# Optimization experiments

Hardware: AMD Instinct MI355X
Metric: run time of the kernel (lower is better)

The kernel has to match this reference:

```python
import jax, jax.numpy as jnp
import numpy as np

B, S, H = 2, 2048, 2048
NH, NKV, HD = 16, 8, 128        # head_dim = H // NH
WINDOW = 1024                    # sliding window size
THETA = 100000.0                 # rope_theta (RotaryEmbedding base)


def setup_inputs() -> dict:
    key = jax.random.key(0)
    ks = jax.random.split(key, 5)
    hidden = jax.random.normal(ks[0], (B, S, H), jnp.float32)
    # fused QKV projection: [H, NH*HD + 2*NKV*HD]
    W_pack = jax.random.normal(ks[1], (H, NH * HD + 2 * NKV * HD), jnp.float32) * (H ** -0.5)
    W_o = jax.random.normal(ks[2], (NH * HD, H), jnp.float32) * ((NH * HD) ** -0.5)
    # per-KV-head 2-tap causal conv weights, softmax-normalized (as in nn.Parameter init)
    conv_k = jax.nn.softmax(jax.random.normal(ks[3], (NKV, 2), jnp.float32), axis=-1)
    conv_v = jax.nn.softmax(jax.random.normal(ks[4], (NKV, 2), jnp.float32), axis=-1)
    return {"hidden": hidden, "W_pack": W_pack, "W_o": W_o, "conv_k": conv_k, "conv_v": conv_v}


def _rope(x, cos, sin):
    # x: (b, s, h, d); cos/sin: (s, d//2); non-interleaved (rotate-half) form
    d2 = x.shape[-1] // 2
    x1, x2 = x[..., :d2], x[..., d2:]
    c = cos[None, :, None, :]
    s = sin[None, :, None, :]
    return jnp.concatenate([x1 * c - x2 * s, x2 * c + x1 * s], axis=-1)


def _causal_conv2(x, w):
    # x: (b, s, kv, d); w: (kv, 2). out[t] = w0*x[t-1] + w1*x[t], zero-padded at t=0
    x_prev = jnp.pad(x, ((0, 0), (1, 0), (0, 0), (0, 0)))[:, :-1]
    return w[None, None, :, 0:1] * x_prev + w[None, None, :, 1:2] * x


def reference(hidden, W_pack, W_o, conv_k, conv_v):
    b, s, _ = hidden.shape
    qkv = hidden @ W_pack                                  # (b, s, NH*HD + 2*NKV*HD)
    q = qkv[..., : NH * HD].reshape(b, s, NH, HD)
    k = qkv[..., NH * HD : NH * HD + NKV * HD].reshape(b, s, NKV, HD)
    v = qkv[..., NH * HD + NKV * HD :].reshape(b, s, NKV, HD)

    inv_freq = 1.0 / (THETA ** (jnp.arange(0, HD, 2, dtype=jnp.float32) / HD))
    freqs = jnp.outer(jnp.arange(s, dtype=jnp.float32), inv_freq)  # (s, HD/2)
    cos, sin = jnp.cos(freqs), jnp.sin(freqs)
    q = _rope(q, cos, sin)
    k = _rope(k, cos, sin)

    # learned 2-tap causal conv mixing adjacent K/V states, per KV head
    k = _causal_conv2(k, conv_k)
    v = _causal_conv2(v, conv_v)

    # GQA: repeat kv heads to match query heads
    group = NH // NKV
    k = jnp.repeat(k, group, axis=2)  # (b, s, NH, HD)
    v = jnp.repeat(v, group, axis=2)

    scores = jnp.einsum('bqhd,bkhd->bhqk', q, k) / jnp.sqrt(jnp.float32(HD))
    i = jnp.arange(s)[:, None]
    j = jnp.arange(s)[None, :]
    mask = (j <= i) & (i - j < WINDOW)  # causal sliding-window mask
    scores = jnp.where(mask[None, None], scores, jnp.finfo(scores.dtype).min)
    probs = jax.nn.softmax(scores, axis=-1)
    out = jnp.einsum('bhqk,bkhd->bqhd', probs, v).reshape(b, s, NH * HD)
    return out @ W_o
```

## Files before the change

kernel.cpp:

```cpp
#include <hip/hip_runtime.h>

#define DI __device__ __forceinline__

typedef unsigned short u16;
typedef __attribute__((ext_vector_type(8))) short s16x8;
typedef __attribute__((ext_vector_type(8))) unsigned short u16x8;
typedef __attribute__((ext_vector_type(4))) float f32x4;
typedef __attribute__((ext_vector_type(16))) float f32x16;

DI u16 f2bf(float x) {
  union { float f; unsigned u; } a; a.f = x;
  unsigned r = a.u + 0x7FFFu + ((a.u >> 16) & 1u);
  return (u16)(r >> 16);
}
DI float bf2f(u16 u) {
  union { unsigned u; float f; } a; a.u = ((unsigned)u) << 16;
  return a.f;
}
DI void gload16(const void* g, void* l) {
  __builtin_amdgcn_global_load_lds(
      (const __attribute__((address_space(1))) unsigned int*)g,
      (__attribute__((address_space(3))) unsigned int*)l, 16, 0, 0);
}
DI f32x4 mfma16(s16x8 a, s16x8 b, f32x4 c) {
  return __builtin_amdgcn_mfma_f32_16x16x32_bf16(a, b, c, 0, 0, 0);
}
DI f32x16 mfma32(s16x8 a, s16x8 b, f32x16 c) {
  return __builtin_amdgcn_mfma_f32_32x32x16_bf16(a, b, c, 0, 0, 0);
}

DI void store4(u16* p, f32x4 v) {
  union { u16 u[4]; unsigned long long ll; } o;
  o.u[0] = f2bf(v[0]); o.u[1] = f2bf(v[1]); o.u[2] = f2bf(v[2]); o.u[3] = f2bf(v[3]);
  *(unsigned long long*)p = o.ll;
}
DI void store4(float* p, f32x4 v) { *(f32x4*)p = v; }

#define SBAR() asm volatile("s_barrier" ::: "memory")

__global__ __launch_bounds__(256) void prep_kernel(
    const float* __restrict__ hidden, const float* __restrict__ W_pack,
    const float* __restrict__ W_o, u16* __restrict__ hA, u16* __restrict__ wpT,
    u16* __restrict__ woT, float* __restrict__ cosT, float* __restrict__ sinT) {
  int bi = blockIdx.x;
  int t = threadIdx.x;
  if (bi < 4096) {
    int i = bi * 256 + t;
    const float4* p = (const float4*)hidden + (size_t)i * 2;
    float4 a = p[0], b = p[1];
    u16x8 o;
    o[0] = f2bf(a.x); o[1] = f2bf(a.y); o[2] = f2bf(a.z); o[3] = f2bf(a.w);
    o[4] = f2bf(b.x); o[5] = f2bf(b.y); o[6] = f2bf(b.z); o[7] = f2bf(b.w);
    *((u16x8*)hA + i) = o;
  } else if (bi < 7168) {
    const float* W; u16* Wt; int R, C, c0, r0;
    if (bi < 6144) {
      int idx = bi - 4096;
      W = W_pack; Wt = wpT; R = 2048; C = 4096;
      c0 = (idx & 63) * 64; r0 = (idx >> 6) * 64;
    } else {
      int idx = bi - 6144;
      W = W_o; Wt = woT; R = 2048; C = 2048;
      c0 = (idx & 31) * 64; r0 = (idx >> 5) * 64;
    }
    __shared__ u16 tile[64][65];
#pragma unroll
    for (int i = 0; i < 16; ++i) {
      int flat = i * 256 + t;
      int r = flat >> 6, c = flat & 63;
      tile[r][c] = f2bf(W[(size_t)(r0 + r) * C + (c0 + c)]);
    }
    __syncthreads();
#pragma unroll
    for (int i = 0; i < 16; ++i) {
      int flat = i * 256 + t;
      int c = flat >> 6, r = flat & 63;
      Wt[(size_t)(c0 + c) * R + (r0 + r)] = tile[r][c];
    }
  } else {
    int i = (bi - 7168) * 256 + t;
    int s = i >> 6, d = i & 63;
    float inv = expf(-(float)d * (11.5129254649702295f / 64.f));
    float f = (float)s * inv;
    cosT[i] = cosf(f);
    sinT[i] = sinf(f);
  }
}

__global__ __launch_bounds__(512, 2) void gemm_ring_kernel(
    const u16* __restrict__ A, const u16* __restrict__ Bt, u16* __restrict__ C,
    int M, int N, int K) {
  constexpr int BSZ = 32768;
  __shared__ __align__(16) char lds[4 * BSZ];
  int nwg = gridDim.x, bid = blockIdx.x;
  int cpx = nwg >> 3;
  int swz = (bid & 7) * cpx + (bid >> 3);
  int ntn = N >> 8;
  int bm = swz / ntn, bn = swz - bm * ntn;
  int m0 = bm << 8, n0 = bn << 8;
  int t = threadIdx.x, w = t >> 6, l = t & 63;
  int wm = w >> 2, wn = w & 3;
  int NT = K >> 5;

  unsigned srcA[2], srcB[2];
  unsigned scol = (unsigned)(((t & 3) ^ ((t >> 3) & 3)) << 4);
#pragma unroll
  for (int u = 0; u < 2; ++u) {
    srcA[u] = (unsigned)(m0 + u * 128 + (t >> 2)) * (unsigned)(K * 2) + scol;
    srcB[u] = (unsigned)(n0 + u * 128 + (t >> 2)) * (unsigned)(K * 2) + scol;
  }
  unsigned dstT = (unsigned)(t * 16);
  const char* Ab = (const char*)A;
  const char* Bb = (const char*)Bt;

#define STAGE(tile) do { int _t = (tile); if (_t < NT) {                        \
    char* _bb = lds + (size_t)(_t & 3) * BSZ;                                    \
    unsigned _k = (unsigned)_t * 64u;                                            \
    gload16(Ab + (size_t)(srcA[0] + _k), _bb + dstT);                            \
    gload16(Ab + (size_t)(srcA[1] + _k), _bb + 8192 + dstT);                     \
    gload16(Bb + (size_t)(srcB[0] + _k), _bb + 16384 + dstT);                    \
    gload16(Bb + (size_t)(srcB[1] + _k), _bb + 24576 + dstT);                    \
  } } while (0)

  int lanemix = ((l & 15) << 6) + ((((l >> 4) ^ ((l >> 1) & 3))) << 4);

  f32x4 acc[8][4] = {};
  s16x8 af[8], bfr[4];

  STAGE(0); STAGE(1); STAGE(2);
  asm volatile("s_waitcnt vmcnt(8)" ::: "memory");
  SBAR();

  for (int tt = 0; tt < NT; ++tt) {
    char* buf = lds + (size_t)(tt & 3) * BSZ;
    const char* Ard = buf + wm * 8192 + lanemix;
    const char* Brd = buf + 16384 + wn * 4096 + lanemix;
    STAGE(tt + 3);
#pragma unroll
    for (int mf = 0; mf < 8; ++mf) af[mf] = *(const s16x8*)(Ard + mf * 1024);
#pragma unroll
    for (int nf = 0; nf < 4; ++nf) bfr[nf] = *(const s16x8*)(Brd + nf * 1024);
    __builtin_amdgcn_s_setprio(1);
#pragma unroll
    for (int mf = 0; mf < 8; ++mf)
#pragma unroll
      for (int nf = 0; nf < 4; ++nf)
        acc[mf][nf] = mfma16(bfr[nf], af[mf], acc[mf][nf]);
    __builtin_amdgcn_s_setprio(0);
    if (tt + 1 < NT) {
      if (tt + 3 < NT)      asm volatile("s_waitcnt vmcnt(8)" ::: "memory");
      else if (tt + 2 < NT) asm volatile("s_waitcnt vmcnt(4)" ::: "memory");
      else                  asm volatile("s_waitcnt vmcnt(0)" ::: "memory");
      SBAR();
    }
  }
#undef STAGE

#pragma unroll
  for (int mf = 0; mf < 8; ++mf) {
    int row = m0 + wm * 128 + mf * 16 + (l & 15);
    u16* crow = C + (size_t)row * N + n0 + wn * 64 + (l >> 4) * 4;
#pragma unroll
    for (int nf = 0; nf < 4; ++nf) store4(crow + nf * 16, acc[mf][nf]);
  }
}

__global__ __launch_bounds__(512, 2) void gemm2r_kernel(
    const u16* __restrict__ A, const u16* __restrict__ Bt, float* __restrict__ C,
    int M, int N, int K) {
  __shared__ __align__(16) char lds[3 * 49152];
  int nwg = gridDim.x, bid = blockIdx.x;
  int cpx = nwg >> 3;
  int swz = (bid & 7) * cpx + (bid >> 3);
  int ntn = N >> 7;
  int bm = swz / ntn, bn = swz - bm * ntn;
  int m0 = bm << 8, n0 = bn << 7;
  int t = threadIdx.x, w = t >> 6, l = t & 63;
  int wm = w >> 2, wn = w & 3;
  int NT = K >> 6;

  unsigned offA[4], offB[2];
  int cA[4], cB[2];
#pragma unroll
  for (int u = 0; u < 4; ++u) {
    int c = u * 8 + w;
    cA[u] = c;
    int d = c * 1024 + l * 16;
    int s = d ^ ((((d >> 7) & 7)) << 4);
    offA[u] = (unsigned)(m0 + (s >> 7)) * (unsigned)(K * 2) + (unsigned)(s & 127);
  }
#pragma unroll
  for (int u = 0; u < 2; ++u) {
    int c = u * 8 + w;
    cB[u] = c;
    int d = c * 1024 + l * 16;
    int s = d ^ ((((d >> 7) & 7)) << 4);
    offB[u] = (unsigned)(n0 + (s >> 7)) * (unsigned)(K * 2) + (unsigned)(s & 127);
  }
  const char* Ab = (const char*)A;
  const char* Bb = (const char*)Bt;

#define STG(tile) do { int _t = (tile); if (_t < NT) {                          \
    char* _bb = lds + (size_t)(_t % 3) * 49152;                                  \
    unsigned _k = (unsigned)_t * 128u;                                           \
    gload16(Ab + (size_t)(offA[0] + _k), _bb + cA[0] * 1024);                    \
    gload16(Ab + (size_t)(offA[1] + _k), _bb + cA[1] * 1024);                    \
    gload16(Ab + (size_t)(offA[2] + _k), _bb + cA[2] * 1024);                    \
    gload16(Ab + (size_t)(offA[3] + _k), _bb + cA[3] * 1024);                    \
    gload16(Bb + (size_t)(offB[0] + _k), _bb + 32768 + cB[0] * 1024);            \
    gload16(Bb + (size_t)(offB[1] + _k), _bb + 32768 + cB[1] * 1024);            \
  } } while (0)

  int lanemix = ((l & 15) << 7) + ((((l >> 4) << 4) ^ ((l & 7) << 4)));
  int lanemix1 = lanemix ^ 64;

  f32x4 acc[8][2] = {};
  s16x8 af[8][2], bf0[2], bf1[2];

  STG(0); STG(1);
  asm volatile("s_waitcnt vmcnt(6)" ::: "memory");
  SBAR();

  for (int tt = 0; tt < NT; ++tt) {
    char* buf = lds + (size_t)(tt % 3) * 49152;
    const char* Ard0 = buf + (wm << 14) + lanemix;
    const char* Ard1 = buf + (wm << 14) + lanemix1;
    const char* Brd0 = buf + 32768 + (wn << 12) + lanemix;
    const char* Brd1 = buf + 32768 + (wn << 12) + lanemix1;
    STG(tt + 2);
#pragma unroll
    for (int mf = 0; mf < 8; ++mf) {
      af[mf][0] = *(const s16x8*)(Ard0 + mf * 2048);
      af[mf][1] = *(const s16x8*)(Ard1 + mf * 2048);
    }
    bf0[0] = *(const s16x8*)(Brd0);
    bf0[1] = *(const s16x8*)(Brd1);
    bf1[0] = *(const s16x8*)(Brd0 + 2048);
    bf1[1] = *(const s16x8*)(Brd1 + 2048);
    __builtin_amdgcn_s_setprio(1);
#pragma unroll
    for (int mf = 0; mf < 8; ++mf) {
      acc[mf][0] = mfma16(bf0[0], af[mf][0], acc[mf][0]);
      acc[mf][0] = mfma16(bf0[1], af[mf][1], acc[mf][0]);
      acc[mf][1] = mfma16(bf1[0], af[mf][0], acc[mf][1]);
      acc[mf][1] = mfma16(bf1[1], af[mf][1], acc[mf][1]);
    }
    __builtin_amdgcn_s_setprio(0);
    if (tt + 1 < NT) {
      if (tt + 2 < NT) asm volatile("s_waitcnt vmcnt(6)" ::: "memory");
      else             asm volatile("s_waitcnt vmcnt(0)" ::: "memory");
      SBAR();
    }
  }
#undef STG

#pragma unroll
  for (int mf = 0; mf < 8; ++mf) {
    int row = m0 + wm * 128 + mf * 16 + (l & 15);
    float* crow = C + (size_t)row * N + n0 + wn * 32 + (l >> 4) * 4;
#pragma unroll
    for (int nf = 0; nf < 2; ++nf) store4(crow + nf * 16, acc[mf][nf]);
  }
}

__global__ void rcvt_kernel(const u16* __restrict__ qkv, const float* __restrict__ cosT,
                            const float* __restrict__ sinT, const float* __restrict__ convk,
                            const float* __restrict__ convv,
                            u16* __restrict__ kb, u16* __restrict__ vt) {
  int t = threadIdx.x;
  if (blockIdx.x < 4096) {
    int row = blockIdx.x;
    int b = row >> 11, s = row & 2047;
    const u16* kr = qkv + (size_t)row * 4096 + 2048;
#pragma unroll
    for (int i = 0; i < 2; ++i) {
      int p = i * 256 + t;
      int h = p >> 6, d = p & 63;
      float c = cosT[s * 64 + d], sn = sinT[s * 64 + d];
      float x1 = bf2f(kr[h * 128 + d]), x2 = bf2f(kr[h * 128 + 64 + d]);
      float r1 = x1 * c - x2 * sn, r2 = x2 * c + x1 * sn;
      float p1 = 0.f, p2 = 0.f;
      if (s > 0) {
        const u16* kp = kr - 4096;
        float cp = cosT[(s - 1) * 64 + d], sp = sinT[(s - 1) * 64 + d];
        float y1 = bf2f(kp[h * 128 + d]), y2 = bf2f(kp[h * 128 + 64 + d]);
        p1 = y1 * cp - y2 * sp;
        p2 = y2 * cp + y1 * sp;
      }
      float w0 = convk[h * 2], w1 = convk[h * 2 + 1];
      size_t o = (((size_t)b * 8 + h) * 2048 + s) * 128;
      kb[o + d] = f2bf(w0 * p1 + w1 * r1);
      kb[o + 64 + d] = f2bf(w0 * p2 + w1 * r2);
    }
  } else {
    __shared__ u16 lt[128][72];
    int idx = blockIdx.x - 4096;
    int st = idx & 31, bh = idx >> 5;
    int b = bh >> 3, h = bh & 7;
    int s0 = st * 64;
    float w0 = convv[h * 2], w1 = convv[h * 2 + 1];
#pragma unroll
    for (int i = 0; i < 32; ++i) {
      int flat = i * 256 + t;
      int sl = flat >> 7, d = flat & 127;
      int s = s0 + sl;
      int row = b * 2048 + s;
      float x = bf2f(qkv[(size_t)row * 4096 + 3072 + h * 128 + d]);
      float xp = (s > 0) ? bf2f(qkv[(size_t)(row - 1) * 4096 + 3072 + h * 128 + d]) : 0.f;
      lt[d][sl] = f2bf(w0 * xp + w1 * x);
    }
    __syncthreads();
#pragma unroll
    for (int i = 0; i < 32; ++i) {
      int flat = i * 256 + t;
      int d = flat >> 6, sl = flat & 63;
      vt[((size_t)(b * 8 + h) * 128 + d) * 2048 + s0 + sl] = lt[d][sl];
    }
  }
}

__global__ __launch_bounds__(256, 2) void attn2_kernel(
    const u16* __restrict__ qkv, const float* __restrict__ cosT,
    const float* __restrict__ sinT, const u16* __restrict__ kbuf,
    const u16* __restrict__ vt, u16* __restrict__ ao) {
  __shared__ __align__(16) char lds[65536];
  int qt = blockIdx.x, bh = blockIdx.y;
  int b = bh >> 4, h = bh & 15, kh = h >> 1;
  int t = threadIdx.x, w = t >> 6, l = t & 63;
  int i0 = qt * 128;
  int qbase = i0 + w * 32;
  int lq = l & 31, hi = l >> 5;
  int xorc = (l & 7) << 4;
  const char* Kg = (const char*)(kbuf + (size_t)(b * 8 + kh) * 2048 * 128);
  const char* Vg = (const char*)(vt + (size_t)(b * 8 + kh) * 128 * 2048);

  s16x8 qf[8];
  {
    const float qs = 0.08838834764831845f;
    int srow = qbase + lq;
    const u16* qp = qkv + ((size_t)(b * 2048 + srow)) * 4096 + h * 128 + 8 * hi;
    const float* cb = cosT + srow * 64 + 8 * hi;
    const float* sb = sinT + srow * 64 + 8 * hi;
#pragma unroll
    for (int kc = 0; kc < 4; ++kc) {
      s16x8 vlo = *(const s16x8*)(qp + kc * 16);
      s16x8 vhi = *(const s16x8*)(qp + 64 + kc * 16);
      float4 c0 = *(const float4*)(cb + kc * 16);
      float4 c1 = *(const float4*)(cb + kc * 16 + 4);
      float4 s0 = *(const float4*)(sb + kc * 16);
      float4 s1 = *(const float4*)(sb + kc * 16 + 4);
      float cc[8] = {c0.x, c0.y, c0.z, c0.w, c1.x, c1.y, c1.z, c1.w};
      float ss[8] = {s0.x, s0.y, s0.z, s0.w, s1.x, s1.y, s1.z, s1.w};
      u16 ol[8], oh[8];
#pragma unroll
      for (int j = 0; j < 8; ++j) {
        float xl = bf2f(((const u16*)&vlo)[j]);
        float xh = bf2f(((const u16*)&vhi)[j]);
        ol[j] = f2bf((xl * cc[j] - xh * ss[j]) * qs);
        oh[j] = f2bf((xh * cc[j] + xl * ss[j]) * qs);
      }
      qf[kc] = *(s16x8*)ol;
      qf[kc + 4] = *(s16x8*)oh;
    }
  }

  unsigned ksrc[4], vsrc[4], kdst[4], vdst[4];
#pragma unroll
  for (int i = 0; i < 4; ++i) {
    int c = w * 4 + i;
    int row = c * 4 + (l >> 4);
    int colb = (l & 15) * 16;
    ksrc[i] = (unsigned)(row * 256 + (colb ^ ((row & 7) << 4)));
    kdst[i] = (unsigned)(c * 1024);
    int d = c * 8 + (l >> 3);
    int cb2 = (l & 7) * 16;
    vsrc[i] = (unsigned)(d * 4096 + (cb2 ^ ((d & 7) << 4)));
    vdst[i] = (unsigned)(16384 + c * 1024);
  }

#define STAGEKV(tile, buf) do { int _j2 = (tile) << 6;                          \
    char* _lb = lds + ((buf) << 15);                                             \
    const char* _ks = Kg + (size_t)_j2 * 256;                                    \
    const char* _vs = Vg + (size_t)_j2 * 2;                                      \
    gload16(_ks + ksrc[0], _lb + kdst[0]); gload16(_vs + vsrc[0], _lb + vdst[0]);\
    gload16(_ks + ksrc[1], _lb + kdst[1]); gload16(_vs + vsrc[1], _lb + vdst[1]);\
    gload16(_ks + ksrc[2], _lb + kdst[2]); gload16(_vs + vsrc[2], _lb + vdst[2]);\
    gload16(_ks + ksrc[3], _lb + kdst[3]); gload16(_vs + vsrc[3], _lb + vdst[3]);\
  } while (0)

  int lo = i0 - 1023; if (lo < 0) lo = 0;
  int tk0 = lo >> 6, tk1 = (i0 + 127) >> 6;

  f32x16 acco[4] = {};
  float ls0 = 0.f, ls1 = 0.f, ls2 = 0.f, ls3 = 0.f;

  int cur = 0;
  STAGEKV(tk0, 0);
  asm volatile("s_waitcnt vmcnt(0)" ::: "memory");
  SBAR();

  for (int tk = tk0; tk <= tk1; ++tk) {
    int j0 = tk << 6;
    if (tk < tk1) STAGEKV(tk + 1, cur ^ 1);
    bool relevant = (j0 <= qbase + 31) && (j0 + 63 >= qbase - 1023);
    if (relevant) {
      const char* Kl = lds + (cur << 15);
      const char* Vl = Kl + 16384;
      const char* Krow = Kl + lq * 256;
      f32x16 ps0 = {}, ps1 = {};
      __builtin_amdgcn_s_setprio(1);
#pragma unroll
      for (int kc = 0; kc < 8; ++kc) {
        s16x8 kf = *(const s16x8*)(Krow + ((kc * 32 + hi * 16) ^ xorc));
        ps0 = mfma32(kf, qf[kc], ps0);
      }
#pragma unroll
      for (int kc = 0; kc < 8; ++kc) {
        s16x8 kf = *(const s16x8*)(Krow + 8192 + ((kc * 32 + hi * 16) ^ xorc));
        ps1 = mfma32(kf, qf[kc], ps1);
      }
      __builtin_amdgcn_s_setprio(0);
      bool domask = (j0 + 63 > qbase) || (qbase + 31 - j0 >= 1024);
      int di0 = qbase + lq - j0;
      float pe[32];
#pragma unroll
      for (int r = 0; r < 16; ++r) {
        float s0 = ps0[r], s1 = ps1[r];
        if (domask) {
          int crow = (r & 3) + 8 * (r >> 2) + 4 * hi;
          if ((unsigned)(di0 - crow) >= 1024u) s0 = -1e30f;
          if ((unsigned)(di0 - 32 - crow) >= 1024u) s1 = -1e30f;
        }
        float e0 = __expf(s0), e1 = __expf(s1);
        pe[r] = e0; pe[16 + r] = e1;
        if ((r & 3) == 0) { ls0 += e0 + e1; }
        else if ((r & 3) == 1) { ls1 += e0 + e1; }
        else if ((r & 3) == 2) { ls2 += e0 + e1; }
        else { ls3 += e0 + e1; }
      }
      unsigned pk[16];
#pragma unroll
      for (int p = 0; p < 16; ++p) {
        asm("v_cvt_pk_bf16_f32 %0, %1, %2" : "=v"(pk[p]) : "v"(pe[2 * p]), "v"(pe[2 * p + 1]));
      }
      s16x8 pa[4];
#pragma unroll
      for (int ks = 0; ks < 4; ++ks) {
        int base = (ks >> 1) * 8 + (ks & 1) * 4;
        unsigned keep0 = hi ? pk[base + 2] : pk[base + 0];
        unsigned keep1 = hi ? pk[base + 3] : pk[base + 1];
        unsigned send0 = hi ? pk[base + 0] : pk[base + 2];
        unsigned send1 = hi ? pk[base + 1] : pk[base + 3];
        unsigned recv0 = (unsigned)__shfl_xor((int)send0, 32);
        unsigned recv1 = (unsigned)__shfl_xor((int)send1, 32);
        union { unsigned u[4]; s16x8 v; } pu;
        pu.u[0] = hi ? recv0 : keep0;
        pu.u[1] = hi ? recv1 : keep1;
        pu.u[2] = hi ? keep0 : recv0;
        pu.u[3] = hi ? keep1 : recv1;
        pa[ks] = pu.v;
      }
      __builtin_amdgcn_s_setprio(1);
#pragma unroll
      for (int db = 0; db < 4; ++db) {
        const char* Vrow = Vl + db * 4096 + lq * 128;
#pragma unroll
        for (int ks = 0; ks < 4; ++ks) {
          s16x8 vf = *(const s16x8*)(Vrow + ((ks * 32 + hi * 16) ^ xorc));
          acco[db] = mfma32(pa[ks], vf, acco[db]);
        }
      }
      __builtin_amdgcn_s_setprio(0);
    }
    asm volatile("s_waitcnt vmcnt(0)" ::: "memory");
    SBAR();
    cur ^= 1;
  }
#undef STAGEKV

  float lrow = (ls0 + ls1) + (ls2 + ls3);
  float lt2 = lrow + __shfl_xor(lrow, 32);
  float rinv = 1.f / lt2;
#pragma unroll
  for (int r = 0; r < 16; ++r) {
    int qidx = (r & 3) + 8 * (r >> 2) + 4 * hi;
    float rv = __shfl(rinv, qidx);
    int i = qbase + qidx;
    u16* orow = ao + ((size_t)(b * 2048 + i)) * 2048 + h * 128 + lq;
#pragma unroll
    for (int db = 0; db < 4; ++db)
      orow[db * 32] = f2bf(acco[db][r] * rv);
  }
}

extern "C" void kernel_launch(void* const* d_in, const int* in_sizes, int n_in,
                              void* d_out, int out_size, void* d_ws, size_t ws_size,
                              hipStream_t stream) {
  (void)in_sizes; (void)n_in; (void)out_size; (void)ws_size;
  const float* hidden = (const float*)d_in[0];
  const float* W_pack = (const float*)d_in[1];
  const float* W_o    = (const float*)d_in[2];
  const float* conv_k = (const float*)d_in[3];
  const float* conv_v = (const float*)d_in[4];

  char* ws = (char*)d_ws;
  const size_t MB = 1u << 20;
  u16* hA    = (u16*)(ws + 0);
  u16* wpT   = (u16*)(ws + 16 * MB);
  u16* woT   = (u16*)(ws + 32 * MB);
  u16* qkv   = (u16*)(ws + 40 * MB);
  u16* attnb = (u16*)(ws + 72 * MB);
  u16* kbuf  = (u16*)(ws + 88 * MB);
  u16* vtb   = (u16*)(ws + 96 * MB);
  float* cosT = (float*)(ws + 104 * MB);
  float* sinT = (float*)(ws + 104 * MB + 524288);

  prep_kernel<<<7680, 256, 0, stream>>>(hidden, W_pack, W_o, hA, wpT, woT, cosT, sinT);
  gemm_ring_kernel<<<256, 512, 0, stream>>>(hA, wpT, qkv, 4096, 4096, 2048);
  rcvt_kernel<<<4608, 256, 0, stream>>>(qkv, cosT, sinT, conv_k, conv_v, kbuf, vtb);
  attn2_kernel<<<dim3(16, 32), 256, 0, stream>>>(qkv, cosT, sinT, kbuf, vtb, attnb);
  gemm2r_kernel<<<256, 512, 0, stream>>>(attnb, woT, (float*)d_out, 4096, 2048, 2048);
}
```

Before: 192.3 us.

## Replace output-projection GEMM with 128x128 tile, double-buffered, 256-thread kernel

```diff
diff --git a/kernel.cpp b/kernel.cpp
--- a/kernel.cpp
+++ b/kernel.cpp
@@ -165,101 +165,78 @@
   }
 }
 
-__global__ __launch_bounds__(512, 2) void gemm2r_kernel(
+__global__ __launch_bounds__(256) void gemm97_kernel(
     const u16* __restrict__ A, const u16* __restrict__ Bt, float* __restrict__ C,
     int M, int N, int K) {
-  __shared__ __align__(16) char lds[3 * 49152];
+  __shared__ __align__(16) char lds[32768];
   int nwg = gridDim.x, bid = blockIdx.x;
   int cpx = nwg >> 3;
   int swz = (bid & 7) * cpx + (bid >> 3);
   int ntn = N >> 7;
   int bm = swz / ntn, bn = swz - bm * ntn;
-  int m0 = bm << 8, n0 = bn << 7;
+  int m0 = bm << 7, n0 = bn << 7;
   int t = threadIdx.x, w = t >> 6, l = t & 63;
-  int wm = w >> 2, wn = w & 3;
-  int NT = K >> 6;
-
-  unsigned offA[4], offB[2];
-  int cA[4], cB[2];
-#pragma unroll
-  for (int u = 0; u < 4; ++u) {
-    int c = u * 8 + w;
-    cA[u] = c;
-    int d = c * 1024 + l * 16;
-    int s = d ^ ((((d >> 7) & 7)) << 4);
-    offA[u] = (unsigned)(m0 + (s >> 7)) * (unsigned)(K * 2) + (unsigned)(s & 127);
-  }
+  int wm = w >> 1, wn = w & 1;
+  int NT = K >> 5;
+
+  unsigned srcA[2], srcB[2];
+  unsigned scol = (unsigned)(((t & 3) ^ ((t >> 3) & 3)) << 4);
 #pragma unroll
   for (int u = 0; u < 2; ++u) {
-    int c = u * 8 + w;
-    cB[u] = c;
-    int d = c * 1024 + l * 16;
-    int s = d ^ ((((d >> 7) & 7)) << 4);
-    offB[u] = (unsigned)(n0 + (s >> 7)) * (unsigned)(K * 2) + (unsigned)(s & 127);
-  }
+    srcA[u] = (unsigned)(m0 + u * 64 + (t >> 2)) * (unsigned)(K * 2) + scol;
+    srcB[u] = (unsigned)(n0 + u * 64 + (t >> 2)) * (unsigned)(K * 2) + scol;
+  }
+  unsigned dstT = (unsigned)(t * 16);
   const char* Ab = (const char*)A;
   const char* Bb = (const char*)Bt;
 
-#define STG(tile) do { int _t = (tile); if (_t < NT) {                          \
-    char* _bb = lds + (size_t)(_t % 3) * 49152;                                  \
-    unsigned _k = (unsigned)_t * 128u;                                           \
-    gload16(Ab + (size_t)(offA[0] + _k), _bb + cA[0] * 1024);                    \
-    gload16(Ab + (size_t)(offA[1] + _k), _bb + cA[1] * 1024);                    \
-    gload16(Ab + (size_t)(offA[2] + _k), _bb + cA[2] * 1024);                    \
-    gload16(Ab + (size_t)(offA[3] + _k), _bb + cA[3] * 1024);                    \
-    gload16(Bb + (size_t)(offB[0] + _k), _bb + 32768 + cB[0] * 1024);            \
-    gload16(Bb + (size_t)(offB[1] + _k), _bb + 32768 + cB[1] * 1024);            \
+#define STG97(tile) do { int _t = (tile); if (_t < NT) {                        \
+    char* _bb = lds + ((_t & 1) << 14);                                          \
+    unsigned _k = (unsigned)_t * 64u;                                            \
+    gload16(Ab + (size_t)(srcA[0] + _k), _bb + dstT);                            \
+    gload16(Ab + (size_t)(srcA[1] + _k), _bb + 4096 + dstT);                     \
+    gload16(Bb + (size_t)(srcB[0] + _k), _bb + 8192 + dstT);                     \
+    gload16(Bb + (size_t)(srcB[1] + _k), _bb + 12288 + dstT);                    \
   } } while (0)
 
-  int lanemix = ((l & 15) << 7) + ((((l >> 4) << 4) ^ ((l & 7) << 4)));
-  int lanemix1 = lanemix ^ 64;
-
-  f32x4 acc[8][2] = {};
-  s16x8 af[8][2], bf0[2], bf1[2];
-
-  STG(0); STG(1);
-  asm volatile("s_waitcnt vmcnt(6)" ::: "memory");
+  int lanemix = ((l & 15) << 6) + ((((l >> 4) ^ ((l >> 1) & 3))) << 4);
+
+  f32x4 acc[4][4] = {};
+  s16x8 af[4], bfr[4];
+
+  STG97(0);
+  asm volatile("s_waitcnt vmcnt(0)" ::: "memory");
   SBAR();
 
   for (int tt = 0; tt < NT; ++tt) {
-    char* buf = lds + (size_t)(tt % 3) * 49152;
-    const char* Ard0 = buf + (wm << 14) + lanemix;
-    const char* Ard1 = buf + (wm << 14) + lanemix1;
-    const char* Brd0 = buf + 32768 + (wn << 12) + lanemix;
-    const char* Brd1 = buf + 32768 + (wn << 12) + lanemix1;
-    STG(tt + 2);
-#pragma unroll
-    for (int mf = 0; mf < 8; ++mf) {
-      af[mf][0] = *(const s16x8*)(Ard0 + mf * 2048);
-      af[mf][1] = *(const s16x8*)(Ard1 + mf * 2048);
-    }
-    bf0[0] = *(const s16x8*)(Brd0);
-    bf0[1] = *(const s16x8*)(Brd1);
-    bf1[0] = *(const s16x8*)(Brd0 + 2048);
-    bf1[1] = *(const s16x8*)(Brd1 + 2048);
+    const char* buf = lds + ((tt & 1) << 14);
+    const char* Ard = buf + wm * 4096 + lanemix;
+    const char* Brd = buf + 8192 + wn * 4096 + lanemix;
+    STG97(tt + 1);
+#pragma unroll
+    for (int mf = 0; mf < 4; ++mf) af[mf] = *(const s16x8*)(Ard + mf * 1024);
+#pragma unroll
+    for (int nf = 0; nf < 4; ++nf) bfr[nf] = *(const s16x8*)(Brd + nf * 1024);
     __builtin_amdgcn_s_setprio(1);
 #pragma unroll
-    for (int mf = 0; mf < 8; ++mf) {
-      acc[mf][0] = mfma16(bf0[0], af[mf][0], acc[mf][0]);
-      acc[mf][0] = mfma16(bf0[1], af[mf][1], acc[mf][0]);
-      acc[mf][1] = mfma16(bf1[0], af[mf][0], acc[mf][1]);
-      acc[mf][1] = mfma16(bf1[1], af[mf][1], acc[mf][1]);
-    }
+    for (int mf = 0; mf < 4; ++mf)
+#pragma unroll
+      for (int nf = 0; nf < 4; ++nf)
+        acc[mf][nf] = mfma16(bfr[nf], af[mf], acc[mf][nf]);
     __builtin_amdgcn_s_setprio(0);
     if (tt + 1 < NT) {
-      if (tt + 2 < NT) asm volatile("s_waitcnt vmcnt(6)" ::: "memory");
-      else             asm volatile("s_waitcnt vmcnt(0)" ::: "memory");
+      asm volatile("s_waitcnt vmcnt(0)" ::: "memory");
       SBAR();
     }
   }
-#undef STG
-
-#pragma unroll
-  for (int mf = 0; mf < 8; ++mf) {
-    int row = m0 + wm * 128 + mf * 16 + (l & 15);
-    float* crow = C + (size_t)row * N + n0 + wn * 32 + (l >> 4) * 4;
-#pragma unroll
-    for (int nf = 0; nf < 2; ++nf) store4(crow + nf * 16, acc[mf][nf]);
+#undef STG97
+
+#pragma unroll
+  for (int mf = 0; mf < 4; ++mf) {
+    int row = m0 + wm * 64 + mf * 16 + (l & 15);
+    float* crow = C + (size_t)row * N + n0 + wn * 64 + (l >> 4) * 4;
+#pragma unroll
+    for (int nf = 0; nf < 4; ++nf) store4(crow + nf * 16, acc[mf][nf]);
   }
 }
 
@@ -519,5 +496,5 @@
   gemm_ring_kernel<<<256, 512, 0, stream>>>(hA, wpT, qkv, 4096, 4096, 2048);
   rcvt_kernel<<<4608, 256, 0, stream>>>(qkv, cosT, sinT, conv_k, conv_v, kbuf, vtb);
   attn2_kernel<<<dim3(16, 32), 256, 0, stream>>>(qkv, cosT, sinT, kbuf, vtb, attnb);
-  gemm2r_kernel<<<256, 512, 0, stream>>>(attnb, woT, (float*)d_out, 4096, 2048, 2048);
-}
+  gemm97_kernel<<<512, 256, 0, stream>>>(attnb, woT, (float*)d_out, 4096, 2048, 2048);
+}
```

Measured after the change: 194.8 us. About the same (+1.3%).
